# Optimization experiments

Measured on AMD Instinct MI355X. Metric: run time of the kernel, lower is better.

The kernel has to match this reference:

```python
import jax, jax.numpy as jnp
import numpy as np

MASK_VALUE = 0.0  # default `mask=0` scalar in the original forward


def setup_inputs() -> dict:
    key = jax.random.key(0)
    kq, kk, kv = jax.random.split(key, 3)
    b, n, d_k, d_v = 8, 2048, 64, 64
    q = jax.random.normal(kq, (b, n, d_k), dtype=jnp.float32)
    k = jax.random.normal(kk, (b, n, d_k), dtype=jnp.float32)
    v = jax.random.normal(kv, (b, n, d_v), dtype=jnp.float32)
    return {"q": q, "k": k, "v": v}


def reference(q, k, v):
    d_k = q.shape[-1]
    temper = jnp.asarray(d_k, q.dtype) ** 0.5
    # scores: (b, n, n)
    attn = jnp.einsum('bqd,bkd->bqk', q, k) / temper
    # equality-based masking: positions whose score exactly equals the
    # scalar `mask` (default 0) are set to -inf before softmax.
    attn = jnp.where(attn == MASK_VALUE, -jnp.inf, attn)
    # NOTE: the original code calls `attn.masked_fill(look_ahead_mask==0, -inf)`
    # WITHOUT assignment, so the look-ahead mask is a no-op; we omit it faithfully.
    attn = jax.nn.softmax(attn, axis=-1)
    out = jnp.einsum('bqk,bkd->bqd', attn, v)  # (b, n, d_v)
    return out
```

## Files before the change

kernel.cpp:

```cpp
#include <hip/hip_runtime.h>
#include <hip/hip_bf16.h>

typedef __bf16 bf16_t;
typedef bf16_t bf16x2 __attribute__((ext_vector_type(2)));
typedef bf16_t bf16x4 __attribute__((ext_vector_type(4)));
typedef bf16_t bf16x8 __attribute__((ext_vector_type(8)));
typedef float  floatx4  __attribute__((ext_vector_type(4)));
typedef float  floatx16 __attribute__((ext_vector_type(16)));

constexpr int B = 8, N = 2048, D = 64;
constexpr int TSTR = 65;

__global__ __launch_bounds__(256)
void prepass_kernel(const float* __restrict__ k, const float* __restrict__ v,
                    bf16_t* __restrict__ kb, bf16_t* __restrict__ vt) {
    __shared__ float t[64 * TSTR];
    const int tid = threadIdx.x;
    const int b   = blockIdx.x & 7;
    const int r0  = ((blockIdx.x >> 3) & 31) * 64;
    if ((blockIdx.x >> 8) == 0) {
        const float* src = k + ((size_t)b * N + r0) * D;
        bf16_t* dst = kb + ((size_t)b * N + r0) * D;
        #pragma unroll
        for (int p = 0; p < 4; ++p) {
            int e = (tid + p * 256) * 4;
            floatx4 f = *(const floatx4*)(src + e);
            bf16x4 o;
            #pragma unroll
            for (int j = 0; j < 4; ++j) o[j] = (bf16_t)f[j];
            *(bf16x4*)(dst + e) = o;
        }
    } else {
        const float* vb = v + ((size_t)b * N + r0) * D;
        #pragma unroll
        for (int p = 0; p < 4; ++p) {
            int e = (tid + p * 256) * 4;
            int row = e >> 6, col = e & 63;
            floatx4 f = *(const floatx4*)(vb + e);
            #pragma unroll
            for (int j = 0; j < 4; ++j) t[(col + j) * TSTR + row] = f[j];
        }
        __syncthreads();
        bf16_t* ob = vt + (size_t)b * D * N + r0;
        #pragma unroll
        for (int p = 0; p < 4; ++p) {
            int e = (tid + p * 256) * 4;
            int drow = e >> 6, kcol = e & 63;
            bf16x4 o;
            #pragma unroll
            for (int j = 0; j < 4; ++j) o[j] = (bf16_t)t[drow * TSTR + kcol + j];
            *(bf16x4*)(ob + (size_t)drow * N + kcol) = o;
        }
    }
}

__global__ __launch_bounds__(512, 4)
void attn_kernel(const float* __restrict__ q, const bf16_t* __restrict__ kb,
                 const bf16_t* __restrict__ vt, float* __restrict__ out) {
    __shared__ char smem[65536];
    bf16_t* lds_k = (bf16_t*)smem;
    bf16_t* lds_v = (bf16_t*)(smem + 32768);
    float*  o_buf = (float*)smem;
    float*  l_buf = (float*)(smem + 57344);

    const int tid  = threadIdx.x;
    const int lane = tid & 63;
    const int cg   = tid >> 6;
    const int h    = lane >> 5;
    const int l31  = lane & 31;
    const int sw   = l31 & 7;

    const int b  = blockIdx.x & 7;
    const int q0 = (blockIdx.x >> 3) * 32;

    const bf16_t* kbb = kb + (size_t)b * N * D;
    const bf16_t* vbb = vt + (size_t)b * D * N;

    bf16x8 qf[4];
    {
        const float* qp = q + ((size_t)b * N + q0 + l31) * D + h * 8;
        #pragma unroll
        for (int kd = 0; kd < 4; ++kd) {
            floatx4 f0 = *(const floatx4*)(qp + kd * 16);
            floatx4 f1 = *(const floatx4*)(qp + kd * 16 + 4);
            bf16x8 t;
            #pragma unroll
            for (int j = 0; j < 4; ++j) { t[j] = (bf16_t)f0[j]; t[j + 4] = (bf16_t)f1[j]; }
            qf[kd] = t;
        }
    }

    floatx16 o_acc[2];
    #pragma unroll
    for (int d = 0; d < 2; ++d)
        #pragma unroll
        for (int i = 0; i < 16; ++i) o_acc[d][i] = 0.f;
    float l_run = 0.f;

    bf16x8 kreg[4], vreg[4];
    #pragma unroll
    for (int p = 0; p < 4; ++p) {
        int e = (tid + p * 512) * 8;
        kreg[p] = *(const bf16x8*)(kbb + e);
        vreg[p] = *(const bf16x8*)(vbb + (size_t)(e >> 8) * N + (e & 255));
    }

    #pragma unroll 1
    for (int it = 0; it < N / 256; ++it) {
        __syncthreads();
        #pragma unroll
        for (int p = 0; p < 4; ++p) {
            int e  = (tid + p * 512) * 8;
            int kr = e >> 6, kg = (e >> 3) & 7;
            *(bf16x8*)&lds_k[kr * 64 + ((kg ^ (kr & 7)) << 3)] = kreg[p];
            int vr = e >> 8, vg = (e >> 3) & 31;
            *(bf16x8*)&lds_v[vr * 256 + ((vg ^ (vr & 7)) << 3)] = vreg[p];
        }
        __syncthreads();
        if (it + 1 < N / 256) {
            const int kv1 = (it + 1) * 256;
            #pragma unroll
            for (int p = 0; p < 4; ++p) {
                int e = (tid + p * 512) * 8;
                kreg[p] = *(const bf16x8*)(kbb + (size_t)kv1 * D + e);
                vreg[p] = *(const bf16x8*)(vbb + (size_t)(e >> 8) * N + kv1 + (e & 255));
            }
        }

        floatx16 s;
        #pragma unroll
        for (int i = 0; i < 16; ++i) s[i] = 0.f;
        #pragma unroll
        for (int kd = 0; kd < 4; ++kd) {
            bf16x8 kf = *(const bf16x8*)&lds_k[(cg * 32 + l31) * 64 + (((2 * kd + h) ^ sw) << 3)];
            s = __builtin_amdgcn_mfma_f32_32x32x16_bf16(kf, qf[kd], s, 0, 0, 0);
        }

        int q8[8];
        #pragma unroll
        for (int g = 0; g < 8; ++g) {
            union { int i; bf16x2 h2; } u;
            #pragma unroll
            for (int j = 0; j < 2; ++j) {
                float x = s[2 * g + j] * 0.125f;
                float p = (x == 0.0f) ? 0.0f : __expf(x);
                l_run += p;
                u.h2[j] = (bf16_t)p;
            }
            q8[g] = u.i;
        }

        #pragma unroll
        for (int s2 = 0; s2 < 2; ++s2) {
            int r0 = __shfl_xor(q8[4 * s2 + 0], 32);
            int r1 = __shfl_xor(q8[4 * s2 + 1], 32);
            int r2 = __shfl_xor(q8[4 * s2 + 2], 32);
            int r3 = __shfl_xor(q8[4 * s2 + 3], 32);
            union { int i4[4]; bf16x8 v; } bf;
            bf.i4[0] = h ? r2 : q8[4 * s2 + 0];
            bf.i4[1] = h ? r3 : q8[4 * s2 + 1];
            bf.i4[2] = h ? q8[4 * s2 + 2] : r0;
            bf.i4[3] = h ? q8[4 * s2 + 3] : r1;
            #pragma unroll
            for (int dblk = 0; dblk < 2; ++dblk) {
                bf16x8 va = *(const bf16x8*)&lds_v[(dblk * 32 + l31) * 256 +
                                                   (((cg * 4 + s2 * 2 + h) ^ sw) << 3)];
                o_acc[dblk] = __builtin_amdgcn_mfma_f32_32x32x16_bf16(va, bf.v, o_acc[dblk], 0, 0, 0);
            }
        }
    }

    __syncthreads();

    l_run += __shfl_xor(l_run, 32);

    if (cg > 0) {
        float* ob = o_buf + (size_t)(cg - 1) * 64 * 32;
        #pragma unroll
        for (int dblk = 0; dblk < 2; ++dblk)
            #pragma unroll
            for (int i = 0; i < 16; ++i) {
                const int d = (i & 3) + 8 * (i >> 2) + 4 * h + dblk * 32;
                ob[d * 32 + l31] = o_acc[dblk][i];
            }
        if (h == 0) l_buf[(cg - 1) * 32 + l31] = l_run;
    }
    __syncthreads();
    if (cg == 0) {
        float lsum = l_run;
        #pragma unroll
        for (int gg = 0; gg < 7; ++gg) lsum += l_buf[gg * 32 + l31];
        const float inv_l = 1.0f / lsum;
        float* op = out + ((size_t)b * N + q0 + l31) * D;
        #pragma unroll
        for (int dblk = 0; dblk < 2; ++dblk)
            #pragma unroll
            for (int g = 0; g < 4; ++g) {
                const int d0 = 8 * g + 4 * h + dblk * 32;
                floatx4 o4;
                #pragma unroll
                for (int j = 0; j < 4; ++j) {
                    float sum = o_acc[dblk][4 * g + j];
                    #pragma unroll
                    for (int gg = 0; gg < 7; ++gg)
                        sum += o_buf[(size_t)gg * 64 * 32 + (d0 + j) * 32 + l31];
                    o4[j] = sum * inv_l;
                }
                *(floatx4*)(op + d0) = o4;
            }
    }
}

extern "C" void kernel_launch(void* const* d_in, const int* in_sizes, int n_in,
                              void* d_out, int out_size, void* d_ws, size_t ws_size,
                              hipStream_t stream) {
    const float* q = (const float*)d_in[0];
    const float* k = (const float*)d_in[1];
    const float* v = (const float*)d_in[2];
    float* out = (float*)d_out;
    bf16_t* kb = (bf16_t*)d_ws;
    bf16_t* vt = (bf16_t*)((char*)d_ws + (size_t)B * N * D * 2);

    hipLaunchKernelGGL(prepass_kernel, dim3(512), dim3(256), 0, stream, k, v, kb, vt);
    hipLaunchKernelGGL(attn_kernel, dim3(512), dim3(512), 0, stream, q, kb, vt, out);
}
```

Before: 92.64 us.

## Prepack K/V into MFMA fragment layout and load directly into registers

Result: faster. 82.86 us (-10.6%).

```diff
diff --git a/kernel.cpp b/kernel.cpp
--- a/kernel.cpp
+++ b/kernel.cpp
@@ -3,78 +3,68 @@
 
 typedef __bf16 bf16_t;
 typedef bf16_t bf16x2 __attribute__((ext_vector_type(2)));
-typedef bf16_t bf16x4 __attribute__((ext_vector_type(4)));
 typedef bf16_t bf16x8 __attribute__((ext_vector_type(8)));
 typedef float  floatx4  __attribute__((ext_vector_type(4)));
 typedef float  floatx16 __attribute__((ext_vector_type(16)));
 
 constexpr int B = 8, N = 2048, D = 64;
-constexpr int TSTR = 65;
 
 __global__ __launch_bounds__(256)
 void prepass_kernel(const float* __restrict__ k, const float* __restrict__ v,
-                    bf16_t* __restrict__ kb, bf16_t* __restrict__ vt) {
-    __shared__ float t[64 * TSTR];
+                    bf16_t* __restrict__ kf, bf16_t* __restrict__ vf) {
+    __shared__ float t[32 * 65];
     const int tid = threadIdx.x;
     const int b   = blockIdx.x & 7;
-    const int r0  = ((blockIdx.x >> 3) & 31) * 64;
-    if ((blockIdx.x >> 8) == 0) {
-        const float* src = k + ((size_t)b * N + r0) * D;
-        bf16_t* dst = kb + ((size_t)b * N + r0) * D;
-        #pragma unroll
-        for (int p = 0; p < 4; ++p) {
-            int e = (tid + p * 256) * 4;
-            floatx4 f = *(const floatx4*)(src + e);
-            bf16x4 o;
-            #pragma unroll
-            for (int j = 0; j < 4; ++j) o[j] = (bf16_t)f[j];
-            *(bf16x4*)(dst + e) = o;
-        }
-    } else {
-        const float* vb = v + ((size_t)b * N + r0) * D;
-        #pragma unroll
-        for (int p = 0; p < 4; ++p) {
-            int e = (tid + p * 256) * 4;
-            int row = e >> 6, col = e & 63;
-            floatx4 f = *(const floatx4*)(vb + e);
-            #pragma unroll
-            for (int j = 0; j < 4; ++j) t[(col + j) * TSTR + row] = f[j];
-        }
+    const int kvb = blockIdx.x >> 3;
+    const size_t inoff  = ((size_t)b * N + kvb * 32) * D;
+    const size_t outoff = (size_t)(b * 64 + kvb) * 2048;
+
+    {
+        const float* src = k + inoff;
+        floatx4 f0 = *(const floatx4*)(src + tid * 8);
+        floatx4 f1 = *(const floatx4*)(src + tid * 8 + 4);
+        bf16x8 o;
+        #pragma unroll
+        for (int j = 0; j < 4; ++j) { o[j] = (bf16_t)f0[j]; o[j + 4] = (bf16_t)f1[j]; }
+        const int rr = tid >> 3, kd = (tid >> 1) & 3, hh = tid & 1;
+        *(bf16x8*)(kf + outoff + (size_t)kd * 512 + (hh * 32 + rr) * 8) = o;
+    }
+    {
+        const float* src = v + inoff;
+        floatx4 f0 = *(const floatx4*)(src + tid * 8);
+        floatx4 f1 = *(const floatx4*)(src + tid * 8 + 4);
+        const int rr = tid >> 3, cc = (tid & 7) * 8;
+        #pragma unroll
+        for (int j = 0; j < 4; ++j) { t[rr * 65 + cc + j] = f0[j]; t[rr * 65 + cc + 4 + j] = f1[j]; }
         __syncthreads();
-        bf16_t* ob = vt + (size_t)b * D * N + r0;
-        #pragma unroll
-        for (int p = 0; p < 4; ++p) {
-            int e = (tid + p * 256) * 4;
-            int drow = e >> 6, kcol = e & 63;
-            bf16x4 o;
-            #pragma unroll
-            for (int j = 0; j < 4; ++j) o[j] = (bf16_t)t[drow * TSTR + kcol + j];
-            *(bf16x4*)(ob + (size_t)drow * N + kcol) = o;
-        }
+        const int s2 = tid >> 7, dblk = (tid >> 6) & 1, lane = tid & 63;
+        const int hh = lane >> 5, l31 = lane & 31;
+        bf16x8 o;
+        #pragma unroll
+        for (int j = 0; j < 8; ++j)
+            o[j] = (bf16_t)t[(s2 * 16 + hh * 8 + j) * 65 + dblk * 32 + l31];
+        *(bf16x8*)(vf + outoff + (size_t)(s2 * 2 + dblk) * 512 + lane * 8) = o;
     }
 }
 
 __global__ __launch_bounds__(512, 4)
-void attn_kernel(const float* __restrict__ q, const bf16_t* __restrict__ kb,
-                 const bf16_t* __restrict__ vt, float* __restrict__ out) {
-    __shared__ char smem[65536];
-    bf16_t* lds_k = (bf16_t*)smem;
-    bf16_t* lds_v = (bf16_t*)(smem + 32768);
-    float*  o_buf = (float*)smem;
-    float*  l_buf = (float*)(smem + 57344);
+void attn_kernel(const float* __restrict__ q, const bf16_t* __restrict__ kf,
+                 const bf16_t* __restrict__ vf, float* __restrict__ out) {
+    __shared__ char smem[58240];
+    float* o_buf = (float*)smem;
+    float* l_buf = (float*)(smem + 57344);
 
     const int tid  = threadIdx.x;
     const int lane = tid & 63;
     const int cg   = tid >> 6;
     const int h    = lane >> 5;
     const int l31  = lane & 31;
-    const int sw   = l31 & 7;
 
     const int b  = blockIdx.x & 7;
     const int q0 = (blockIdx.x >> 3) * 32;
 
-    const bf16_t* kbb = kb + (size_t)b * N * D;
-    const bf16_t* vbb = vt + (size_t)b * D * N;
+    const bf16_t* kfb = kf + (size_t)b * 131072;
+    const bf16_t* vfb = vf + (size_t)b * 131072;
 
     bf16x8 qf[4];
     {
@@ -97,44 +87,37 @@
         for (int i = 0; i < 16; ++i) o_acc[d][i] = 0.f;
     float l_run = 0.f;
 
-    bf16x8 kreg[4], vreg[4];
+    bf16x8 kreg[4];
     #pragma unroll
-    for (int p = 0; p < 4; ++p) {
-        int e = (tid + p * 512) * 8;
-        kreg[p] = *(const bf16x8*)(kbb + e);
-        vreg[p] = *(const bf16x8*)(vbb + (size_t)(e >> 8) * N + (e & 255));
-    }
+    for (int kd = 0; kd < 4; ++kd)
+        kreg[kd] = *(const bf16x8*)(kfb + (size_t)cg * 2048 + kd * 512 + lane * 8);
 
     #pragma unroll 1
-    for (int it = 0; it < N / 256; ++it) {
-        __syncthreads();
-        #pragma unroll
-        for (int p = 0; p < 4; ++p) {
-            int e  = (tid + p * 512) * 8;
-            int kr = e >> 6, kg = (e >> 3) & 7;
-            *(bf16x8*)&lds_k[kr * 64 + ((kg ^ (kr & 7)) << 3)] = kreg[p];
-            int vr = e >> 8, vg = (e >> 3) & 31;
-            *(bf16x8*)&lds_v[vr * 256 + ((vg ^ (vr & 7)) << 3)] = vreg[p];
-        }
-        __syncthreads();
-        if (it + 1 < N / 256) {
-            const int kv1 = (it + 1) * 256;
-            #pragma unroll
-            for (int p = 0; p < 4; ++p) {
-                int e = (tid + p * 512) * 8;
-                kreg[p] = *(const bf16x8*)(kbb + (size_t)kv1 * D + e);
-                vreg[p] = *(const bf16x8*)(vbb + (size_t)(e >> 8) * N + kv1 + (e & 255));
-            }
+    for (int it = 0; it < 8; ++it) {
+        const size_t base = (size_t)(it * 8 + cg) * 2048;
+
+        bf16x8 vreg[4];
+        #pragma unroll
+        for (int u = 0; u < 4; ++u)
+            vreg[u] = *(const bf16x8*)(vfb + base + (size_t)u * 512 + lane * 8);
+
+        bf16x8 kcur[4];
+        #pragma unroll
+        for (int kd = 0; kd < 4; ++kd) kcur[kd] = kreg[kd];
+
+        if (it + 1 < 8) {
+            const size_t nbase = (size_t)((it + 1) * 8 + cg) * 2048;
+            #pragma unroll
+            for (int kd = 0; kd < 4; ++kd)
+                kreg[kd] = *(const bf16x8*)(kfb + nbase + (size_t)kd * 512 + lane * 8);
         }
 
         floatx16 s;
         #pragma unroll
         for (int i = 0; i < 16; ++i) s[i] = 0.f;
         #pragma unroll
-        for (int kd = 0; kd < 4; ++kd) {
-            bf16x8 kf = *(const bf16x8*)&lds_k[(cg * 32 + l31) * 64 + (((2 * kd + h) ^ sw) << 3)];
-            s = __builtin_amdgcn_mfma_f32_32x32x16_bf16(kf, qf[kd], s, 0, 0, 0);
-        }
+        for (int kd = 0; kd < 4; ++kd)
+            s = __builtin_amdgcn_mfma_f32_32x32x16_bf16(kcur[kd], qf[kd], s, 0, 0, 0);
 
         int q8[8];
         #pragma unroll
@@ -162,20 +145,16 @@
             bf.i4[2] = h ? q8[4 * s2 + 2] : r0;
             bf.i4[3] = h ? q8[4 * s2 + 3] : r1;
             #pragma unroll
-            for (int dblk = 0; dblk < 2; ++dblk) {
-                bf16x8 va = *(const bf16x8*)&lds_v[(dblk * 32 + l31) * 256 +
-                                                   (((cg * 4 + s2 * 2 + h) ^ sw) << 3)];
-                o_acc[dblk] = __builtin_amdgcn_mfma_f32_32x32x16_bf16(va, bf.v, o_acc[dblk], 0, 0, 0);
-            }
-        }
-    }
-
-    __syncthreads();
+            for (int dblk = 0; dblk < 2; ++dblk)
+                o_acc[dblk] = __builtin_amdgcn_mfma_f32_32x32x16_bf16(vreg[s2 * 2 + dblk], bf.v,
+                                                                      o_acc[dblk], 0, 0, 0);
+        }
+    }
 
     l_run += __shfl_xor(l_run, 32);
 
     if (cg > 0) {
-        float* ob = o_buf + (size_t)(cg - 1) * 64 * 32;
+        float* ob = o_buf + (size_t)(cg - 1) * 2048;
         #pragma unroll
         for (int dblk = 0; dblk < 2; ++dblk)
             #pragma unroll
@@ -203,7 +182,7 @@
                     float sum = o_acc[dblk][4 * g + j];
                     #pragma unroll
                     for (int gg = 0; gg < 7; ++gg)
-                        sum += o_buf[(size_t)gg * 64 * 32 + (d0 + j) * 32 + l31];
+                        sum += o_buf[(size_t)gg * 2048 + (d0 + j) * 32 + l31];
                     o4[j] = sum * inv_l;
                 }
                 *(floatx4*)(op + d0) = o4;
@@ -218,9 +197,9 @@
     const float* k = (const float*)d_in[1];
     const float* v = (const float*)d_in[2];
     float* out = (float*)d_out;
-    bf16_t* kb = (bf16_t*)d_ws;
-    bf16_t* vt = (bf16_t*)((char*)d_ws + (size_t)B * N * D * 2);
-
-    hipLaunchKernelGGL(prepass_kernel, dim3(512), dim3(256), 0, stream, k, v, kb, vt);
-    hipLaunchKernelGGL(attn_kernel, dim3(512), dim3(512), 0, stream, q, kb, vt, out);
+    bf16_t* kfrag = (bf16_t*)d_ws;
+    bf16_t* vfrag = (bf16_t*)((char*)d_ws + (size_t)B * N * D * 2);
+
+    hipLaunchKernelGGL(prepass_kernel, dim3(512), dim3(256), 0, stream, k, v, kfrag, vfrag);
+    hipLaunchKernelGGL(attn_kernel, dim3(512), dim3(512), 0, stream, q, kfrag, vfrag, out);
 }
```
